# Kernel optimization log

Measured on AMD Instinct MI355X. Metric: run time of the kernel, lower is better.

## Reference

```python
import jax, jax.numpy as jnp
import numpy as np

# Dimensions (LRA BigBird base-ish config)
B, S, D = 4, 4096, 512
H, DH = 8, 64          # num_heads, head_dim = qkv_dim // num_heads
M = 2048               # mlp_dim
BS = 64                # block_size
NB = S // BS           # number of blocks = 64
R = 3                  # num random blocks per row (BigBird default)
K = 8                  # max gathered key blocks per row: 3 window + 2 global + 3 random
SEED = 0               # connectivity_seed
LN_EPS = 1e-6


def _block_indices():
    """Static BigBird connectivity for interior query blocks (rows 1..NB-2).

    Each interior block attends to: window {i-1,i,i+1}, globals {0, NB-1},
    and R random blocks (seeded, disjoint from window/global). Rows where
    window overlaps globals have fewer unique blocks and are padded+masked.
    """
    rng = np.random.RandomState(SEED)
    idx = np.zeros((NB - 2, K), np.int32)
    msk = np.zeros((NB - 2, K), bool)
    for row, i in enumerate(range(1, NB - 1)):
        fixed = sorted({0, NB - 1, i - 1, i, i + 1})
        allowed = [b for b in range(NB) if b not in fixed]
        rand = rng.choice(allowed, size=R, replace=False).tolist()
        blocks = fixed + rand
        idx[row, :len(blocks)] = blocks
        msk[row, :len(blocks)] = True
    return jnp.asarray(idx), jnp.asarray(msk)

IDX, KMASK = _block_indices()  # [NB-2, K] int32 / bool
NEG = -1e9


def _ln(x, scale, bias):
    mu = jnp.mean(x, axis=-1, keepdims=True)
    var = jnp.mean(jnp.square(x - mu), axis=-1, keepdims=True)
    return (x - mu) * jax.lax.rsqrt(var + LN_EPS) * scale + bias


def setup_inputs() -> dict:
    key = jax.random.key(0)
    ks = jax.random.split(key, 7)

    def xav(k, shape, fan_in, fan_out):
        lim = float(np.sqrt(6.0 / (fan_in + fan_out)))
        return jax.random.uniform(k, shape, jnp.float32, -lim, lim)

    return {
        "inputs": jax.random.normal(ks[0], (B, S, D), jnp.float32),
        "ln1_scale": jnp.ones((D,), jnp.float32),
        "ln1_bias": jnp.zeros((D,), jnp.float32),
        "wq": xav(ks[1], (D, H, DH), D, DH),
        "wk": xav(ks[2], (D, H, DH), D, DH),
        "wv": xav(ks[3], (D, H, DH), D, DH),
        "wo": xav(ks[4], (H, DH, D), D, D),
        "ln2_scale": jnp.ones((D,), jnp.float32),
        "ln2_bias": jnp.zeros((D,), jnp.float32),
        "w1": xav(ks[5], (D, M), D, M),
        "b1": jnp.zeros((M,), jnp.float32),
        "w2": xav(ks[6], (M, D), M, D),
        "b2": jnp.zeros((D,), jnp.float32),
    }


def reference(inputs, ln1_scale, ln1_bias, wq, wk, wv, wo,
              ln2_scale, ln2_bias, w1, b1, w2, b2):
    x = _ln(inputs, ln1_scale, ln1_bias)
    scale = 1.0 / jnp.sqrt(jnp.asarray(DH, x.dtype))
    q = jnp.einsum("bsd,dhk->bshk", x, wq) * scale
    k = jnp.einsum("bsd,dhk->bshk", x, wk)
    v = jnp.einsum("bsd,dhk->bshk", x, wv)

    # block layout: [B, H, NB, BS, DH]
    qb = q.reshape(B, NB, BS, H, DH).transpose(0, 3, 1, 2, 4)
    kb = k.reshape(B, NB, BS, H, DH).transpose(0, 3, 1, 2, 4)
    vb = v.reshape(B, NB, BS, H, DH).transpose(0, 3, 1, 2, 4)

    # ---- interior query blocks: sparse (window + global + random) keys ----
    q_int = qb[:, :, 1:NB - 1]                       # [B,H,NB-2,BS,DH]
    k_sel = kb[:, :, IDX]                            # [B,H,NB-2,K,BS,DH]
    v_sel = vb[:, :, IDX]
    s = jnp.einsum("bhnqd,bhnkjd->bhnqkj", q_int, k_sel)
    s = jnp.where(KMASK[None, None, :, None, :, None], s, NEG)
    p = jax.nn.softmax(s.reshape(B, H, NB - 2, BS, K * BS), axis=-1)
    p = p.reshape(B, H, NB - 2, BS, K, BS)
    o_int = jnp.einsum("bhnqkj,bhnkjd->bhnqd", p, v_sel)

    # ---- global query blocks (first & last): full attention ----
    q_g = qb[:, :, jnp.array([0, NB - 1])]           # [B,H,2,BS,DH]
    kf = k.transpose(0, 2, 1, 3)                     # [B,H,S,DH]
    vf = v.transpose(0, 2, 1, 3)
    sg = jnp.einsum("bhgqd,bhtd->bhgqt", q_g, kf)
    pg = jax.nn.softmax(sg, axis=-1)
    o_g = jnp.einsum("bhgqt,bhtd->bhgqd", pg, vf)

    o = jnp.concatenate([o_g[:, :, :1], o_int, o_g[:, :, 1:]], axis=2)
    o = o.transpose(0, 2, 3, 1, 4).reshape(B, S, H, DH)
    attn = jnp.einsum("bshd,hde->bse", o, wo)        # output proj, no bias

    x = attn + inputs                                 # residual 1
    y = _ln(x, ln2_scale, ln2_bias)
    y = jax.nn.gelu(jnp.einsum("bsd,dm->bsm", y, w1) + b1)
    y = jnp.einsum("bsm,md->bsd", y, w2) + b2
    return x + y                                      # residual 2
```

## Files before the change

kernel.cpp:

```cpp
#include <hip/hip_runtime.h>
#include <cstdint>
#include <cstddef>

typedef __bf16 bf16;
typedef __bf16 bf16x8 __attribute__((ext_vector_type(8)));
typedef float  f32x4  __attribute__((ext_vector_type(4)));

#define DEVINL static __device__ __forceinline__

DEVINL void gl2lds16(const void* g, void* l) {
  __builtin_amdgcn_global_load_lds((__attribute__((address_space(1))) void*)g,
                                   (__attribute__((address_space(3))) void*)l,
                                   16, 0, 0);
}

DEVINL float loadf(const void* p, size_t i, int isf) {
  return isf ? ((const float*)p)[i] : (float)((const bf16*)p)[i];
}

DEVINL float gelu_fast(float x) {
  float u = 0.7978845608028654f * (x + 0.044715f * x * x * x);
  float s = 1.f / (1.f + __expf(-2.f * u));
  return x * s;
}

struct TabArg { unsigned char idx[62][8]; unsigned char cnt[62]; };

struct HostMT {
  unsigned mt[624]; int mti;
  void seed(unsigned s) {
    mt[0] = s;
    for (int i = 1; i < 624; ++i) mt[i] = 1812433253u * (mt[i-1] ^ (mt[i-1] >> 30)) + (unsigned)i;
    mti = 624;
  }
  unsigned next() {
    if (mti == 624) {
      for (int i = 0; i < 624; ++i) {
        unsigned y = (mt[i] & 0x80000000u) | (mt[(i+1)%624] & 0x7fffffffu);
        unsigned v = mt[(i+397)%624] ^ (y >> 1);
        if (y & 1u) v ^= 0x9908b0dfu;
        mt[i] = v;
      }
      mti = 0;
    }
    unsigned y = mt[mti++];
    y ^= y >> 11; y ^= (y << 7) & 0x9d2c5680u; y ^= (y << 15) & 0xefc60000u; y ^= y >> 18;
    return y;
  }
  unsigned interval(unsigned mx) {
    if (mx == 0) return 0;
    unsigned mask = mx;
    mask |= mask>>1; mask |= mask>>2; mask |= mask>>4; mask |= mask>>8; mask |= mask>>16;
    unsigned v = next() & mask;
    while (v > mx) v = next() & mask;
    return v;
  }
};

static void build_tab(TabArg* t) {
  HostMT rng; rng.seed(0u);
  for (int row = 0; row < 62; ++row) {
    int i = row + 1;
    bool fix[64] = {};
    fix[0] = true; fix[63] = true; fix[i-1] = true; fix[i] = true; fix[i+1] = true;
    int fixed[5]; int nf = 0; int allowed[64]; int na = 0;
    for (int b = 0; b < 64; ++b) { if (fix[b]) fixed[nf++] = b; else allowed[na++] = b; }
    int perm[64];
    for (int j = 0; j < na; ++j) perm[j] = j;
    for (int j = na - 1; j > 0; --j) {
      unsigned kk = rng.interval((unsigned)j);
      int tmp = perm[j]; perm[j] = perm[kk]; perm[kk] = tmp;
    }
    int nb = 0;
    for (int j = 0; j < nf; ++j) t->idx[row][nb++] = (unsigned char)fixed[j];
    for (int j = 0; j < 3;  ++j) t->idx[row][nb++] = (unsigned char)allowed[perm[j]];
    t->cnt[row] = (unsigned char)nb;
    for (int j = nb; j < 8; ++j) t->idx[row][j] = 0;
  }
}

__global__ __launch_bounds__(256) void detect_kernel(const unsigned short* __restrict__ x,
                                                     int* __restrict__ flag) {
  __shared__ int cnt[256];
  int c = 0;
  for (int i = threadIdx.x; i < 8192; i += 256) {
    int e = (x[i] >> 7) & 0xFF;
    if (e >= 0xC6) c++;
  }
  cnt[threadIdx.x] = c;
  __syncthreads();
  for (int s = 128; s > 0; s >>= 1) {
    if (threadIdx.x < s) cnt[threadIdx.x] += cnt[threadIdx.x + s];
    __syncthreads();
  }
  if (threadIdx.x == 0) *flag = (cnt[0] > 32) ? 1 : 0;
}

struct P6 { const void* s[6]; bf16* d[6]; int n[6]; };
__global__ __launch_bounds__(256) void cvt6_kernel(const int* __restrict__ flagp, P6 p) {
  int isf = *flagp;
  int which = blockIdx.x;
  const void* src = p.s[which];
  bf16* dst = p.d[which];
  int n = p.n[which];
  int i8 = threadIdx.x * 8;
  if (i8 >= n) return;
  bf16x8 o;
  if (isf) {
    const float* s = (const float*)src + i8;
    f32x4 a = *(const f32x4*)s;
    f32x4 b = *(const f32x4*)(s + 4);
#pragma unroll
    for (int j = 0; j < 4; ++j) { o[j] = (bf16)a[j]; o[4+j] = (bf16)b[j]; }
  } else {
    o = *(const bf16x8*)((const bf16*)src + i8);
  }
  *(bf16x8*)(dst + i8) = o;
}

struct W6 { const void* in[6]; bf16* out[6]; int R[6], C[6], start[6]; };
__global__ __launch_bounds__(256) void transpose_w6_kernel(const int* __restrict__ flagp, W6 wz) {
  __shared__ __align__(16) bf16 sT[64 * 72];
  int isf = *flagp;
  int which = 0;
#pragma unroll
  for (int i = 1; i < 6; ++i) if ((int)blockIdx.x >= wz.start[i]) which = i;
  const void* in = wz.in[which];
  bf16* out = wz.out[which];
  int R = wz.R[which], C = wz.C[which];
  int bid = blockIdx.x - wz.start[which];
  int cb = C >> 6;
  int br = bid / cb, bc = bid % cb;
  int r0 = br * 64, c0 = bc * 64;
  int t = threadIdx.x;
#pragma unroll
  for (int p = 0; p < 2; ++p) {
    int cid = p * 256 + t;
    int r = cid >> 3, c = cid & 7;
    bf16x8 v;
    if (isf) {
      const float* s = (const float*)in + (size_t)(r0 + r) * C + c0 + c * 8;
      f32x4 a = *(const f32x4*)s;
      f32x4 b = *(const f32x4*)(s + 4);
#pragma unroll
      for (int j = 0; j < 4; ++j) { v[j] = (bf16)a[j]; v[4+j] = (bf16)b[j]; }
    } else {
      v = *(const bf16x8*)((const bf16*)in + (size_t)(r0 + r) * C + c0 + c * 8);
    }
    *(bf16x8*)&sT[r * 72 + c * 8] = v;
  }
  __syncthreads();
#pragma unroll
  for (int p = 0; p < 2; ++p) {
    int cid = p * 256 + t;
    int oc = cid >> 3, rc = cid & 7;
    bf16x8 vv;
#pragma unroll
    for (int i = 0; i < 8; ++i) vv[i] = sT[(rc * 8 + i) * 72 + oc];
    *(bf16x8*)&out[(size_t)(c0 + oc) * R + r0 + rc * 8] = vv;
  }
}

__global__ __launch_bounds__(256) void ln_any_kernel(const int* __restrict__ flagp,
                                                     const void* __restrict__ x,
                                                     const bf16* __restrict__ sc,
                                                     const bf16* __restrict__ bi,
                                                     bf16* __restrict__ out) {
  int isf = *flagp;
  int row  = blockIdx.x * 4 + (threadIdx.x >> 6);
  int lane = threadIdx.x & 63;
  float f[8];
  if (isf) {
    const float* xf = (const float*)x + (size_t)row * 512 + lane * 8;
    f32x4 a = *(const f32x4*)xf;
    f32x4 b = *(const f32x4*)(xf + 4);
#pragma unroll
    for (int j = 0; j < 4; ++j) { f[j] = a[j]; f[4+j] = b[j]; }
  } else {
    bf16x8 v = ((const bf16x8*)((const bf16*)x + (size_t)row * 512))[lane];
#pragma unroll
    for (int j = 0; j < 8; ++j) f[j] = (float)v[j];
  }
  float s = 0.f, s2 = 0.f;
#pragma unroll
  for (int i = 0; i < 8; ++i) { s += f[i]; s2 += f[i]*f[i]; }
#pragma unroll
  for (int o = 32; o > 0; o >>= 1) { s += __shfl_xor(s, o, 64); s2 += __shfl_xor(s2, o, 64); }
  float mu  = s  * (1.f/512.f);
  float var = s2 * (1.f/512.f) - mu*mu;
  float rs  = rsqrtf(fmaxf(var, 0.f) + 1e-6f);
  bf16x8 sv = ((const bf16x8*)sc)[lane];
  bf16x8 bv = ((const bf16x8*)bi)[lane];
  bf16x8 o8;
#pragma unroll
  for (int i = 0; i < 8; ++i) o8[i] = (bf16)((f[i]-mu)*rs*(float)sv[i] + (float)bv[i]);
  ((bf16x8*)(out + (size_t)row * 512))[lane] = o8;
}

__global__ __launch_bounds__(256) void ln_bf16_kernel(const bf16* __restrict__ x,
                                                      const bf16* __restrict__ sc,
                                                      const bf16* __restrict__ bi,
                                                      bf16* __restrict__ out) {
  int row  = blockIdx.x * 4 + (threadIdx.x >> 6);
  int lane = threadIdx.x & 63;
  bf16x8 v = ((const bf16x8*)(x + (size_t)row * 512))[lane];
  float f[8], s = 0.f, s2 = 0.f;
#pragma unroll
  for (int i = 0; i < 8; ++i) { f[i] = (float)v[i]; s += f[i]; s2 += f[i]*f[i]; }
#pragma unroll
  for (int o = 32; o > 0; o >>= 1) { s += __shfl_xor(s, o, 64); s2 += __shfl_xor(s2, o, 64); }
  float mu  = s  * (1.f/512.f);
  float var = s2 * (1.f/512.f) - mu*mu;
  float rs  = rsqrtf(fmaxf(var, 0.f) + 1e-6f);
  bf16x8 sv = ((const bf16x8*)sc)[lane];
  bf16x8 bv = ((const bf16x8*)bi)[lane];
  bf16x8 o8;
#pragma unroll
  for (int i = 0; i < 8; ++i) o8[i] = (bf16)((f[i]-mu)*rs*(float)sv[i] + (float)bv[i]);
  ((bf16x8*)(out + (size_t)row * 512))[lane] = o8;
}

__global__ __launch_bounds__(256) void transpose_v_kernel(const bf16* __restrict__ v,
                                                          bf16* __restrict__ vT) {
  __shared__ __align__(16) bf16 sT[64 * 72];
  int st = blockIdx.x & 63;
  int h  = (blockIdx.x >> 6) & 7;
  int b  = blockIdx.x >> 9;
  int s0 = st * 64;
  int t  = threadIdx.x;
  const size_t ibase = ((size_t)b * 4096) * 512 + h * 64;
#pragma unroll
  for (int p = 0; p < 2; ++p) {
    int cid = p * 256 + t;
    int r = cid >> 3, c = cid & 7;
    *(bf16x8*)&sT[r * 72 + c * 8] = *(const bf16x8*)&v[ibase + (size_t)(s0 + r) * 512 + c * 8];
  }
  __syncthreads();
  const size_t obase = ((size_t)(b * 8 + h) * 64) * 4096;
#pragma unroll
  for (int p = 0; p < 2; ++p) {
    int cid = p * 256 + t;
    int dh = cid >> 3, scn = cid & 7;
    bf16x8 vv;
#pragma unroll
    for (int i = 0; i < 8; ++i) vv[i] = sT[(scn * 8 + i) * 72 + dh];
    *(bf16x8*)&vT[obase + (size_t)dh * 4096 + s0 + scn * 8] = vv;
  }
}

__global__ __launch_bounds__(256) void gemm_kernel(const bf16* __restrict__ A,
                                                   const bf16* __restrict__ BT,
                                                   int M, int N, int K,
                                                   int epi,
                                                   const bf16* __restrict__ bias,
                                                   const void* __restrict__ resid,
                                                   void* __restrict__ gout,
                                                   bf16* __restrict__ out2,
                                                   bf16* __restrict__ out3,
                                                   size_t gout_off,
                                                   const int* __restrict__ flagp) {
  __shared__ __align__(16) bf16 As[128 * 64];
  __shared__ __align__(16) bf16 Bs[128 * 64];
  const int t = threadIdx.x;
  const int w = t >> 6, l = t & 63, quad = l >> 4, l15 = l & 15;
  const int wm = w >> 1, wn = w & 1;
  const int m0 = blockIdx.y * 128, n0 = blockIdx.x * 128;
  const int isf = (epi == 1 || epi == 3) ? *flagp : 0;
  f32x4 acc[4][4] = {};
  const int nk = K >> 6;
  for (int kt = 0; kt < nk; ++kt) {
    __syncthreads();
#pragma unroll
    for (int p = 0; p < 4; ++p) {
      int cid = p * 256 + t;
      int r = cid >> 3, c = cid & 7;
      int sc_ = c ^ (r & 7);
      gl2lds16(A  + (size_t)(m0 + r) * K + kt * 64 + sc_ * 8, (char*)As + cid * 16);
      gl2lds16(BT + (size_t)(n0 + r) * K + kt * 64 + sc_ * 8, (char*)Bs + cid * 16);
    }
    __syncthreads();
#pragma unroll
    for (int ks = 0; ks < 2; ++ks) {
      bf16x8 af[4], bfr[4];
      int cc = ks * 4 + quad;
#pragma unroll
      for (int mt = 0; mt < 4; ++mt) {
        int r = wm * 64 + mt * 16 + l15;
        af[mt] = *(const bf16x8*)&As[r * 64 + ((cc ^ (r & 7)) << 3)];
      }
#pragma unroll
      for (int nt = 0; nt < 4; ++nt) {
        int r = wn * 64 + nt * 16 + l15;
        bfr[nt] = *(const bf16x8*)&Bs[r * 64 + ((cc ^ (r & 7)) << 3)];
      }
#pragma unroll
      for (int mt = 0; mt < 4; ++mt)
#pragma unroll
        for (int nt = 0; nt < 4; ++nt)
          acc[mt][nt] = __builtin_amdgcn_mfma_f32_16x16x32_bf16(af[mt], bfr[nt], acc[mt][nt], 0, 0, 0);
    }
  }
#pragma unroll
  for (int mt = 0; mt < 4; ++mt) {
    int rowb = m0 + wm * 64 + mt * 16 + quad * 4;
#pragma unroll
    for (int nt = 0; nt < 4; ++nt) {
      int col = n0 + wn * 64 + nt * 16 + l15;
#pragma unroll
      for (int r = 0; r < 4; ++r) {
        int row = rowb + r;
        float vacc = acc[mt][nt][r];
        size_t oidx = (size_t)row * N + col;
        if (epi == 5) {
          int which = col >> 9, c2 = col & 511;
          bf16 ov = (bf16)(which == 0 ? vacc * 0.125f : vacc);
          bf16* dst = which == 0 ? (bf16*)gout : (which == 1 ? out2 : out3);
          dst[(size_t)row * 512 + c2] = ov;
        } else if (epi == 1) {
          ((bf16*)gout)[oidx] = (bf16)(vacc + loadf(resid, oidx, isf));
        } else if (epi == 2) {
          ((bf16*)gout)[oidx] = (bf16)gelu_fast(vacc + (float)bias[col]);
        } else {
          float v = vacc + (float)bias[col] + (float)((const bf16*)resid)[oidx];
          if (isf) ((float*)gout)[gout_off + oidx] = v;
          else     ((bf16*)gout)[gout_off + oidx] = (bf16)v;
        }
      }
    }
  }
}

__global__ __launch_bounds__(256) void attn_kernel(TabArg targ,
                                                   const bf16* __restrict__ q,
                                                   const bf16* __restrict__ k,
                                                   const bf16* __restrict__ vT,
                                                   bf16* __restrict__ o,
                                                   float* __restrict__ part,
                                                   int mode) {
  __shared__ __align__(16) bf16 sQ[64 * 64];
  __shared__ __align__(16) bf16 sK[64 * 64];
  __shared__ __align__(16) bf16 sV[64 * 64];
  __shared__ __align__(16) bf16 sP[64 * 64];

  const int t = threadIdx.x;
  const int w = t >> 6, l = t & 63, quad = l >> 4, l15 = l & 15;
  int n, bh, chunk = 0, niter;
  if (mode == 0) {
    n = 1 + (int)(blockIdx.x % 62);
    bh = blockIdx.x / 62;
    niter = (int)targ.cnt[n - 1];
  } else {
    chunk = blockIdx.x & 7;
    int g = (blockIdx.x >> 3) & 1;
    bh = blockIdx.x >> 4;
    n = g ? 63 : 0;
    niter = 8;
  }
  const int b = bh >> 3, h = bh & 7;
  const size_t bh_qk = ((size_t)b * 4096) * 512 + h * 64;
  const size_t bh_v  = ((size_t)(b * 8 + h) * 64) * 4096;

#pragma unroll
  for (int p = 0; p < 2; ++p) {
    int cid = p * 256 + t;
    int r = cid >> 3, c = cid & 7;
    int sc_ = c ^ (r & 7);
    gl2lds16(q + bh_qk + (size_t)(n * 64 + r) * 512 + sc_ * 8, (char*)sQ + cid * 16);
  }

  float m_r[4], l_r[4];
#pragma unroll
  for (int r = 0; r < 4; ++r) { m_r[r] = -1e30f; l_r[r] = 0.f; }
  f32x4 accO[4] = {};

  for (int it = 0; it < niter; ++it) {
    int kb = (mode == 0) ? (int)targ.idx[n - 1][it] : chunk * 8 + it;
    __syncthreads();
#pragma unroll
    for (int p = 0; p < 2; ++p) {
      int cid = p * 256 + t;
      int r = cid >> 3, c = cid & 7;
      int sc_ = c ^ (r & 7);
      gl2lds16(k  + bh_qk + (size_t)(kb * 64 + r) * 512 + sc_ * 8, (char*)sK + cid * 16);
      gl2lds16(vT + bh_v  + (size_t)r * 4096 + kb * 64 + sc_ * 8,  (char*)sV + cid * 16);
    }
    __syncthreads();

    f32x4 accS[4] = {};
#pragma unroll
    for (int ks = 0; ks < 2; ++ks) {
      int rQ = w * 16 + l15;
      int cc = ks * 4 + quad;
      bf16x8 afr = *(const bf16x8*)&sQ[rQ * 64 + ((cc ^ (rQ & 7)) << 3)];
#pragma unroll
      for (int j = 0; j < 4; ++j) {
        int rK = j * 16 + l15;
        bf16x8 bfr = *(const bf16x8*)&sK[rK * 64 + ((cc ^ (rK & 7)) << 3)];
        accS[j] = __builtin_amdgcn_mfma_f32_16x16x32_bf16(afr, bfr, accS[j], 0, 0, 0);
      }
    }

    float al[4];
#pragma unroll
    for (int r = 0; r < 4; ++r) {
      float mx = fmaxf(fmaxf(accS[0][r], accS[1][r]), fmaxf(accS[2][r], accS[3][r]));
#pragma unroll
      for (int off = 1; off < 16; off <<= 1) mx = fmaxf(mx, __shfl_xor(mx, off, 64));
      float mnew = fmaxf(m_r[r], mx);
      al[r] = __expf(m_r[r] - mnew);
      m_r[r] = mnew;
      int rowp = w * 16 + quad * 4 + r;
      float ps = 0.f;
#pragma unroll
      for (int j = 0; j < 4; ++j) {
        float pv = __expf(accS[j][r] - mnew);
        ps += pv;
        int col = j * 16 + l15;
        sP[rowp * 64 + (((col >> 3) ^ (rowp & 7)) << 3) + (col & 7)] = (bf16)pv;
      }
#pragma unroll
      for (int off = 1; off < 16; off <<= 1) ps += __shfl_xor(ps, off, 64);
      l_r[r] = l_r[r] * al[r] + ps;
    }

#pragma unroll
    for (int dt = 0; dt < 4; ++dt)
#pragma unroll
      for (int r = 0; r < 4; ++r) accO[dt][r] *= al[r];
#pragma unroll
    for (int ks = 0; ks < 2; ++ks) {
      int rP = w * 16 + l15;
      int cc = ks * 4 + quad;
      bf16x8 afr = *(const bf16x8*)&sP[rP * 64 + ((cc ^ (rP & 7)) << 3)];
#pragma unroll
      for (int dt = 0; dt < 4; ++dt) {
        int rV = dt * 16 + l15;
        bf16x8 bfr = *(const bf16x8*)&sV[rV * 64 + ((cc ^ (rV & 7)) << 3)];
        accO[dt] = __builtin_amdgcn_mfma_f32_16x16x32_bf16(afr, bfr, accO[dt], 0, 0, 0);
      }
    }
  }

  if (mode == 0) {
#pragma unroll
    for (int r = 0; r < 4; ++r) {
      int qr = w * 16 + quad * 4 + r;
      float linv = 1.f / fmaxf(l_r[r], 1e-30f);
      int srow = n * 64 + qr;
#pragma unroll
      for (int dt = 0; dt < 4; ++dt)
        o[bh_qk + (size_t)srow * 512 + dt * 16 + l15] = (bf16)(accO[dt][r] * linv);
    }
  } else {
    float* pb = part + (size_t)blockIdx.x * (4096 + 128);
#pragma unroll
    for (int r = 0; r < 4; ++r) {
      int row = w * 16 + quad * 4 + r;
#pragma unroll
      for (int dt = 0; dt < 4; ++dt)
        pb[row * 64 + dt * 16 + l15] = accO[dt][r];
      if (l15 == 0) { pb[4096 + row] = m_r[r]; pb[4160 + row] = l_r[r]; }
    }
  }
}

__global__ __launch_bounds__(256) void merge_kernel(const float* __restrict__ part,
                                                    bf16* __restrict__ o) {
  const int SP = 4096 + 128;
  int g = blockIdx.x & 1, bh = blockIdx.x >> 1;
  int b = bh >> 3, h = bh & 7, n = g ? 63 : 0;
  int t = threadIdx.x;
  int row = t >> 2, st = t & 3;
  size_t pb0 = (size_t)(bh * 16 + g * 8) * SP;
  float mc[8], lc[8], M = -1e30f;
#pragma unroll
  for (int c = 0; c < 8; ++c) {
    mc[c] = part[pb0 + (size_t)c * SP + 4096 + row];
    lc[c] = part[pb0 + (size_t)c * SP + 4160 + row];
    M = fmaxf(M, mc[c]);
  }
  float L = 0.f;
  float sc[8];
#pragma unroll
  for (int c = 0; c < 8; ++c) { sc[c] = __expf(mc[c] - M); L += lc[c] * sc[c]; }
  float inv = 1.f / fmaxf(L, 1e-30f);
  f32x4 acc[4] = {};
#pragma unroll
  for (int c = 0; c < 8; ++c) {
    const float* Op = part + pb0 + (size_t)c * SP + row * 64 + st * 16;
    float s = sc[c];
#pragma unroll
    for (int i = 0; i < 4; ++i) {
      f32x4 v = *(const f32x4*)(Op + i * 4);
#pragma unroll
      for (int j = 0; j < 4; ++j) acc[i][j] += v[j] * s;
    }
  }
  size_t obase = ((size_t)b * 4096 + n * 64 + row) * 512 + h * 64 + st * 16;
#pragma unroll
  for (int i = 0; i < 4; ++i)
#pragma unroll
    for (int j = 0; j < 4; ++j)
      o[obase + i * 4 + j] = (bf16)(acc[i][j] * inv);
}

extern "C" void kernel_launch(void* const* d_in, const int* in_sizes, int n_in,
                              void* d_out, int out_size, void* d_ws, size_t ws_size,
                              hipStream_t stream) {
  (void)in_sizes; (void)n_in; (void)out_size;
  const void* inputs = d_in[0];
  const void* ln1s = d_in[1];
  const void* ln1b = d_in[2];
  const void* wq   = d_in[3];
  const void* wk   = d_in[4];
  const void* wv   = d_in[5];
  const void* wo   = d_in[6];
  const void* ln2s = d_in[7];
  const void* ln2b = d_in[8];
  const void* w1   = d_in[9];
  const void* b1   = d_in[10];
  const void* w2   = d_in[11];
  const void* b2   = d_in[12];

  TabArg tab;
  build_tab(&tab);

  char* ws = (char*)d_ws;
  size_t off = 0;
  auto alloc = [&](size_t bytes) -> char* {
    char* p = ws + off; off += (bytes + 255) & ~(size_t)255; return p;
  };
  int*  flag   = (int*)alloc(256);
  bf16* ln1s_c = (bf16*)alloc(512 * 2);
  bf16* ln1b_c = (bf16*)alloc(512 * 2);
  bf16* ln2s_c = (bf16*)alloc(512 * 2);
  bf16* ln2b_c = (bf16*)alloc(512 * 2);
  bf16* b1_c   = (bf16*)alloc(2048 * 2);
  bf16* b2_c   = (bf16*)alloc(512 * 2);
  bf16* wqkvT  = (bf16*)alloc(1536ull * 512 * 2);
  bf16* woT    = (bf16*)alloc(512ull * 512 * 2);
  bf16* w1T    = (bf16*)alloc(512ull * 2048 * 2);
  bf16* w2T    = (bf16*)alloc(2048ull * 512 * 2);
  const size_t SZ = 16384ull * 512 * 2;
  bf16* regA = (bf16*)alloc(SZ);
  bf16* regB = (bf16*)alloc(SZ);
  bf16* regC = (bf16*)alloc(SZ);
  bf16* regD = (bf16*)alloc(SZ);
  size_t base_need = off;
  const size_t H1_BYTES = 16384ull * 2048 * 2;
  bool full_ffn = (ws_size >= base_need + H1_BYTES + 256);
  bf16* h1f = full_ffn ? (bf16*)alloc(H1_BYTES) : nullptr;

  bf16* xln  = regA;
  bf16* qb   = regB;
  bf16* kb   = regC;
  bf16* vb   = regD;
  bf16* vTb  = regA;
  bf16* obuf = regD;
  bf16* xbuf = regA;
  bf16* yln  = regB;
  bf16* h1c  = regC;
  float* part = (float*)d_out;

  detect_kernel<<<1, 256, 0, stream>>>((const unsigned short*)inputs, flag);

  P6 p6;
  p6.s[0]=ln1s; p6.s[1]=ln1b; p6.s[2]=ln2s; p6.s[3]=ln2b; p6.s[4]=b1; p6.s[5]=b2;
  p6.d[0]=ln1s_c; p6.d[1]=ln1b_c; p6.d[2]=ln2s_c; p6.d[3]=ln2b_c; p6.d[4]=b1_c; p6.d[5]=b2_c;
  p6.n[0]=512; p6.n[1]=512; p6.n[2]=512; p6.n[3]=512; p6.n[4]=2048; p6.n[5]=512;
  cvt6_kernel<<<6, 256, 0, stream>>>(flag, p6);

  W6 w6;
  w6.in[0]=wq; w6.in[1]=wk; w6.in[2]=wv; w6.in[3]=wo; w6.in[4]=w1; w6.in[5]=w2;
  w6.out[0]=wqkvT; w6.out[1]=wqkvT+512ull*512; w6.out[2]=wqkvT+1024ull*512;
  w6.out[3]=woT; w6.out[4]=w1T; w6.out[5]=w2T;
  w6.R[0]=512; w6.R[1]=512; w6.R[2]=512; w6.R[3]=512; w6.R[4]=512;  w6.R[5]=2048;
  w6.C[0]=512; w6.C[1]=512; w6.C[2]=512; w6.C[3]=512; w6.C[4]=2048; w6.C[5]=512;
  w6.start[0]=0; w6.start[1]=64; w6.start[2]=128; w6.start[3]=192; w6.start[4]=256; w6.start[5]=512;
  transpose_w6_kernel<<<768, 256, 0, stream>>>(flag, w6);

  ln_any_kernel<<<4096, 256, 0, stream>>>(flag, inputs, ln1s_c, ln1b_c, xln);

  gemm_kernel<<<dim3(12, 128), 256, 0, stream>>>(xln, wqkvT, 16384, 1536, 512, 5,
                                                 nullptr, nullptr, qb, kb, vb, 0, flag);

  transpose_v_kernel<<<2048, 256, 0, stream>>>(vb, vTb);

  attn_kernel<<<1984, 256, 0, stream>>>(tab, qb, kb, vTb, obuf, part, 0);
  attn_kernel<<<512,  256, 0, stream>>>(tab, qb, kb, vTb, obuf, part, 1);
  merge_kernel<<<64,  256, 0, stream>>>(part, obuf);

  gemm_kernel<<<dim3(4, 128), 256, 0, stream>>>(obuf, woT, 16384, 512, 512, 1,
                                                nullptr, inputs, xbuf, nullptr, nullptr, 0, flag);

  ln_bf16_kernel<<<4096, 256, 0, stream>>>(xbuf, ln2s_c, ln2b_c, yln);

  if (full_ffn) {
    gemm_kernel<<<dim3(16, 128), 256, 0, stream>>>(yln, w1T, 16384, 2048, 512, 2,
                                                   b1_c, nullptr, h1f, nullptr, nullptr, 0, flag);
    gemm_kernel<<<dim3(4, 128), 256, 0, stream>>>(h1f, w2T, 16384, 512, 2048, 3,
                                                  b2_c, xbuf, d_out, nullptr, nullptr, 0, flag);
  } else {
    for (int c = 0; c < 4; ++c) {
      const bf16* yc = yln  + (size_t)c * 4096 * 512;
      const bf16* xc = xbuf + (size_t)c * 4096 * 512;
      size_t oo = (size_t)c * 4096 * 512;
      gemm_kernel<<<dim3(16, 32), 256, 0, stream>>>(yc, w1T, 4096, 2048, 512, 2,
                                                    b1_c, nullptr, h1c, nullptr, nullptr, 0, flag);
      gemm_kernel<<<dim3(4, 32), 256, 0, stream>>>(h1c, w2T, 4096, 512, 2048, 3,
                                                   b2_c, xc, d_out, nullptr, nullptr, oo, flag);
    }
  }
}
```

Before: 479.6 us.

## Stage GEMM epilogue through LDS for vectorized stores and XCD-aware block mapping

```diff
diff --git a/kernel.cpp b/kernel.cpp
--- a/kernel.cpp
+++ b/kernel.cpp
@@ -12,10 +12,6 @@
   __builtin_amdgcn_global_load_lds((__attribute__((address_space(1))) void*)g,
                                    (__attribute__((address_space(3))) void*)l,
                                    16, 0, 0);
-}
-
-DEVINL float loadf(const void* p, size_t i, int isf) {
-  return isf ? ((const float*)p)[i] : (float)((const bf16*)p)[i];
 }
 
 DEVINL float gelu_fast(float x) {
@@ -250,7 +246,7 @@
 
 __global__ __launch_bounds__(256) void gemm_kernel(const bf16* __restrict__ A,
                                                    const bf16* __restrict__ BT,
-                                                   int M, int N, int K,
+                                                   int N, int K, int nbn,
                                                    int epi,
                                                    const bf16* __restrict__ bias,
                                                    const void* __restrict__ resid,
@@ -259,12 +255,15 @@
                                                    bf16* __restrict__ out3,
                                                    size_t gout_off,
                                                    const int* __restrict__ flagp) {
-  __shared__ __align__(16) bf16 As[128 * 64];
-  __shared__ __align__(16) bf16 Bs[128 * 64];
+  __shared__ __align__(16) bf16 smem[2 * 128 * 64];
+  bf16* As = smem;
+  bf16* Bs = smem + 128 * 64;
   const int t = threadIdx.x;
   const int w = t >> 6, l = t & 63, quad = l >> 4, l15 = l & 15;
   const int wm = w >> 1, wn = w & 1;
-  const int m0 = blockIdx.y * 128, n0 = blockIdx.x * 128;
+  const int xcd = blockIdx.x & 7, g = blockIdx.x >> 3;
+  const int m0 = (xcd + (g / nbn) * 8) * 128;
+  const int n0 = (g % nbn) * 128;
   const int isf = (epi == 1 || epi == 3) ? *flagp : 0;
   f32x4 acc[4][4] = {};
   const int nk = K >> 6;
@@ -300,30 +299,73 @@
           acc[mt][nt] = __builtin_amdgcn_mfma_f32_16x16x32_bf16(af[mt], bfr[nt], acc[mt][nt], 0, 0, 0);
     }
   }
-#pragma unroll
-  for (int mt = 0; mt < 4; ++mt) {
-    int rowb = m0 + wm * 64 + mt * 16 + quad * 4;
-#pragma unroll
-    for (int nt = 0; nt < 4; ++nt) {
-      int col = n0 + wn * 64 + nt * 16 + l15;
-#pragma unroll
-      for (int r = 0; r < 4; ++r) {
-        int row = rowb + r;
-        float vacc = acc[mt][nt][r];
-        size_t oidx = (size_t)row * N + col;
-        if (epi == 5) {
-          int which = col >> 9, c2 = col & 511;
-          bf16 ov = (bf16)(which == 0 ? vacc * 0.125f : vacc);
-          bf16* dst = which == 0 ? (bf16*)gout : (which == 1 ? out2 : out3);
-          dst[(size_t)row * 512 + c2] = ov;
-        } else if (epi == 1) {
-          ((bf16*)gout)[oidx] = (bf16)(vacc + loadf(resid, oidx, isf));
-        } else if (epi == 2) {
-          ((bf16*)gout)[oidx] = (bf16)gelu_fast(vacc + (float)bias[col]);
+
+  const int ESTR = 144;
+  for (int half = 0; half < 2; ++half) {
+    __syncthreads();
+    if (wm == half) {
+#pragma unroll
+      for (int mt = 0; mt < 4; ++mt) {
+        int lr = mt * 16 + quad * 4;
+#pragma unroll
+        for (int nt = 0; nt < 4; ++nt) {
+          int col = wn * 64 + nt * 16 + l15;
+#pragma unroll
+          for (int r = 0; r < 4; ++r) {
+            float v = acc[mt][nt][r];
+            bf16 ov;
+            if (epi == 5)      ov = (bf16)(((n0 + col) >> 9) == 0 ? v * 0.125f : v);
+            else if (epi == 2) ov = (bf16)gelu_fast(v + (float)bias[n0 + col]);
+            else if (epi == 3) ov = (bf16)(v + (float)bias[n0 + col]);
+            else               ov = (bf16)v;
+            smem[(lr + r) * ESTR + col] = ov;
+          }
+        }
+      }
+    }
+    __syncthreads();
+    int gr0 = m0 + half * 64;
+#pragma unroll
+    for (int it = 0; it < 4; ++it) {
+      int cid = it * 256 + t;
+      int lr  = cid >> 4;
+      int c8  = (cid & 15) * 8;
+      bf16x8 vv = *(const bf16x8*)&smem[lr * ESTR + c8];
+      int grow = gr0 + lr;
+      int gcol = n0 + c8;
+      size_t oidx = (size_t)grow * N + gcol;
+      if (epi == 5) {
+        int which = gcol >> 9, c2 = gcol & 511;
+        bf16* dst = which == 0 ? (bf16*)gout : (which == 1 ? out2 : out3);
+        *(bf16x8*)&dst[(size_t)grow * 512 + c2] = vv;
+      } else if (epi == 1) {
+        bf16x8 ov;
+        if (isf) {
+          const float* rp = (const float*)resid + oidx;
+          f32x4 a = *(const f32x4*)rp, b = *(const f32x4*)(rp + 4);
+#pragma unroll
+          for (int j = 0; j < 4; ++j) { ov[j] = (bf16)((float)vv[j] + a[j]); ov[4+j] = (bf16)((float)vv[4+j] + b[j]); }
         } else {
-          float v = vacc + (float)bias[col] + (float)((const bf16*)resid)[oidx];
-          if (isf) ((float*)gout)[gout_off + oidx] = v;
-          else     ((bf16*)gout)[gout_off + oidx] = (bf16)v;
+          bf16x8 rv = *(const bf16x8*)((const bf16*)resid + oidx);
+#pragma unroll
+          for (int j = 0; j < 8; ++j) ov[j] = (bf16)((float)vv[j] + (float)rv[j]);
+        }
+        *(bf16x8*)&((bf16*)gout)[oidx] = ov;
+      } else if (epi == 2) {
+        *(bf16x8*)&((bf16*)gout)[oidx] = vv;
+      } else {
+        bf16x8 rv = *(const bf16x8*)((const bf16*)resid + oidx);
+        if (isf) {
+          float o0[8];
+#pragma unroll
+          for (int j = 0; j < 8; ++j) o0[j] = (float)vv[j] + (float)rv[j];
+          *(f32x4*)&((float*)gout)[gout_off + oidx]     = *(f32x4*)&o0[0];
+          *(f32x4*)&((float*)gout)[gout_off + oidx + 4] = *(f32x4*)&o0[4];
+        } else {
+          bf16x8 ov;
+#pragma unroll
+          for (int j = 0; j < 8; ++j) ov[j] = (bf16)((float)vv[j] + (float)rv[j]);
+          *(bf16x8*)&((bf16*)gout)[gout_off + oidx] = ov;
         }
       }
     }
@@ -346,8 +388,10 @@
   const int w = t >> 6, l = t & 63, quad = l >> 4, l15 = l & 15;
   int n, bh, chunk = 0, niter;
   if (mode == 0) {
-    n = 1 + (int)(blockIdx.x % 62);
-    bh = blockIdx.x / 62;
+    int xcd = blockIdx.x & 7, g = blockIdx.x >> 3;
+    int bhloc = g / 62;
+    n  = 1 + g % 62;
+    bh = xcd + bhloc * 8;
     niter = (int)targ.cnt[n - 1];
   } else {
     chunk = blockIdx.x & 7;
@@ -581,8 +625,8 @@
 
   ln_any_kernel<<<4096, 256, 0, stream>>>(flag, inputs, ln1s_c, ln1b_c, xln);
 
-  gemm_kernel<<<dim3(12, 128), 256, 0, stream>>>(xln, wqkvT, 16384, 1536, 512, 5,
-                                                 nullptr, nullptr, qb, kb, vb, 0, flag);
+  gemm_kernel<<<128 * 12, 256, 0, stream>>>(xln, wqkvT, 1536, 512, 12, 5,
+                                            nullptr, nullptr, qb, kb, vb, 0, flag);
 
   transpose_v_kernel<<<2048, 256, 0, stream>>>(vb, vTb);
 
@@ -590,25 +634,25 @@
   attn_kernel<<<512,  256, 0, stream>>>(tab, qb, kb, vTb, obuf, part, 1);
   merge_kernel<<<64,  256, 0, stream>>>(part, obuf);
 
-  gemm_kernel<<<dim3(4, 128), 256, 0, stream>>>(obuf, woT, 16384, 512, 512, 1,
-                                                nullptr, inputs, xbuf, nullptr, nullptr, 0, flag);
+  gemm_kernel<<<128 * 4, 256, 0, stream>>>(obuf, woT, 512, 512, 4, 1,
+                                           nullptr, inputs, xbuf, nullptr, nullptr, 0, flag);
 
   ln_bf16_kernel<<<4096, 256, 0, stream>>>(xbuf, ln2s_c, ln2b_c, yln);
 
   if (full_ffn) {
-    gemm_kernel<<<dim3(16, 128), 256, 0, stream>>>(yln, w1T, 16384, 2048, 512, 2,
-                                                   b1_c, nullptr, h1f, nullptr, nullptr, 0, flag);
-    gemm_kernel<<<dim3(4, 128), 256, 0, stream>>>(h1f, w2T, 16384, 512, 2048, 3,
-                                                  b2_c, xbuf, d_out, nullptr, nullptr, 0, flag);
+    gemm_kernel<<<128 * 16, 256, 0, stream>>>(yln, w1T, 2048, 512, 16, 2,
+                                              b1_c, nullptr, h1f, nullptr, nullptr, 0, flag);
+    gemm_kernel<<<128 * 4, 256, 0, stream>>>(h1f, w2T, 512, 2048, 4, 3,
+                                             b2_c, xbuf, d_out, nullptr, nullptr, 0, flag);
   } else {
     for (int c = 0; c < 4; ++c) {
       const bf16* yc = yln  + (size_t)c * 4096 * 512;
       const bf16* xc = xbuf + (size_t)c * 4096 * 512;
       size_t oo = (size_t)c * 4096 * 512;
-      gemm_kernel<<<dim3(16, 32), 256, 0, stream>>>(yc, w1T, 4096, 2048, 512, 2,
-                                                    b1_c, nullptr, h1c, nullptr, nullptr, 0, flag);
-      gemm_kernel<<<dim3(4, 32), 256, 0, stream>>>(h1c, w2T, 4096, 512, 2048, 3,
-                                                   b2_c, xc, d_out, nullptr, nullptr, oo, flag);
-    }
-  }
-}
+      gemm_kernel<<<32 * 16, 256, 0, stream>>>(yc, w1T, 2048, 512, 16, 2,
+                                               b1_c, nullptr, h1c, nullptr, nullptr, 0, flag);
+      gemm_kernel<<<32 * 4, 256, 0, stream>>>(h1c, w2T, 512, 2048, 4, 3,
+                                              b2_c, xc, d_out, nullptr, nullptr, oo, flag);
+    }
+  }
+}
```

After: 485.1 us. No clear change (+1.1%).

## Double-buffer GEMM LDS tiles and remap blocks to group work per XCD

Applied to the files above, without the earlier changes.

```diff
diff --git a/kernel.cpp b/kernel.cpp
--- a/kernel.cpp
+++ b/kernel.cpp
@@ -250,7 +250,7 @@
 
 __global__ __launch_bounds__(256) void gemm_kernel(const bf16* __restrict__ A,
                                                    const bf16* __restrict__ BT,
-                                                   int M, int N, int K,
+                                                   int N, int K, int nbn,
                                                    int epi,
                                                    const bf16* __restrict__ bias,
                                                    const void* __restrict__ resid,
@@ -259,26 +259,43 @@
                                                    bf16* __restrict__ out3,
                                                    size_t gout_off,
                                                    const int* __restrict__ flagp) {
-  __shared__ __align__(16) bf16 As[128 * 64];
-  __shared__ __align__(16) bf16 Bs[128 * 64];
+  __shared__ __align__(16) bf16 As[2][128 * 64];
+  __shared__ __align__(16) bf16 Bs[2][128 * 64];
   const int t = threadIdx.x;
   const int w = t >> 6, l = t & 63, quad = l >> 4, l15 = l & 15;
   const int wm = w >> 1, wn = w & 1;
-  const int m0 = blockIdx.y * 128, n0 = blockIdx.x * 128;
+  const int xcd = blockIdx.x & 7, g = blockIdx.x >> 3;
+  const int m0 = (xcd + (g / nbn) * 8) * 128;
+  const int n0 = (g % nbn) * 128;
   const int isf = (epi == 1 || epi == 3) ? *flagp : 0;
   f32x4 acc[4][4] = {};
   const int nk = K >> 6;
+
+  const int sr = t >> 1;
+  (void)sr;
+
+#pragma unroll
+  for (int p = 0; p < 4; ++p) {
+    int cid = p * 256 + t;
+    int r = cid >> 3, c = cid & 7;
+    int sc_ = c ^ (r & 7);
+    gl2lds16(A  + (size_t)(m0 + r) * K + sc_ * 8, (char*)As[0] + cid * 16);
+    gl2lds16(BT + (size_t)(n0 + r) * K + sc_ * 8, (char*)Bs[0] + cid * 16);
+  }
+
   for (int kt = 0; kt < nk; ++kt) {
     __syncthreads();
-#pragma unroll
-    for (int p = 0; p < 4; ++p) {
-      int cid = p * 256 + t;
-      int r = cid >> 3, c = cid & 7;
-      int sc_ = c ^ (r & 7);
-      gl2lds16(A  + (size_t)(m0 + r) * K + kt * 64 + sc_ * 8, (char*)As + cid * 16);
-      gl2lds16(BT + (size_t)(n0 + r) * K + kt * 64 + sc_ * 8, (char*)Bs + cid * 16);
-    }
-    __syncthreads();
+    int nb = (kt + 1) & 1, cb = kt & 1;
+    if (kt + 1 < nk) {
+#pragma unroll
+      for (int p = 0; p < 4; ++p) {
+        int cid = p * 256 + t;
+        int r = cid >> 3, c = cid & 7;
+        int sc_ = c ^ (r & 7);
+        gl2lds16(A  + (size_t)(m0 + r) * K + (kt + 1) * 64 + sc_ * 8, (char*)As[nb] + cid * 16);
+        gl2lds16(BT + (size_t)(n0 + r) * K + (kt + 1) * 64 + sc_ * 8, (char*)Bs[nb] + cid * 16);
+      }
+    }
 #pragma unroll
     for (int ks = 0; ks < 2; ++ks) {
       bf16x8 af[4], bfr[4];
@@ -286,12 +303,12 @@
 #pragma unroll
       for (int mt = 0; mt < 4; ++mt) {
         int r = wm * 64 + mt * 16 + l15;
-        af[mt] = *(const bf16x8*)&As[r * 64 + ((cc ^ (r & 7)) << 3)];
+        af[mt] = *(const bf16x8*)&As[cb][r * 64 + ((cc ^ (r & 7)) << 3)];
       }
 #pragma unroll
       for (int nt = 0; nt < 4; ++nt) {
         int r = wn * 64 + nt * 16 + l15;
-        bfr[nt] = *(const bf16x8*)&Bs[r * 64 + ((cc ^ (r & 7)) << 3)];
+        bfr[nt] = *(const bf16x8*)&Bs[cb][r * 64 + ((cc ^ (r & 7)) << 3)];
       }
 #pragma unroll
       for (int mt = 0; mt < 4; ++mt)
@@ -300,6 +317,7 @@
           acc[mt][nt] = __builtin_amdgcn_mfma_f32_16x16x32_bf16(af[mt], bfr[nt], acc[mt][nt], 0, 0, 0);
     }
   }
+
 #pragma unroll
   for (int mt = 0; mt < 4; ++mt) {
     int rowb = m0 + wm * 64 + mt * 16 + quad * 4;
@@ -346,8 +364,10 @@
   const int w = t >> 6, l = t & 63, quad = l >> 4, l15 = l & 15;
   int n, bh, chunk = 0, niter;
   if (mode == 0) {
-    n = 1 + (int)(blockIdx.x % 62);
-    bh = blockIdx.x / 62;
+    int xcd = blockIdx.x & 7, g = blockIdx.x >> 3;
+    int bhloc = g / 62;
+    n  = 1 + g % 62;
+    bh = xcd + bhloc * 8;
     niter = (int)targ.cnt[n - 1];
   } else {
     chunk = blockIdx.x & 7;
@@ -581,8 +601,8 @@
 
   ln_any_kernel<<<4096, 256, 0, stream>>>(flag, inputs, ln1s_c, ln1b_c, xln);
 
-  gemm_kernel<<<dim3(12, 128), 256, 0, stream>>>(xln, wqkvT, 16384, 1536, 512, 5,
-                                                 nullptr, nullptr, qb, kb, vb, 0, flag);
+  gemm_kernel<<<128 * 12, 256, 0, stream>>>(xln, wqkvT, 1536, 512, 12, 5,
+                                            nullptr, nullptr, qb, kb, vb, 0, flag);
 
   transpose_v_kernel<<<2048, 256, 0, stream>>>(vb, vTb);
 
@@ -590,25 +610,25 @@
   attn_kernel<<<512,  256, 0, stream>>>(tab, qb, kb, vTb, obuf, part, 1);
   merge_kernel<<<64,  256, 0, stream>>>(part, obuf);
 
-  gemm_kernel<<<dim3(4, 128), 256, 0, stream>>>(obuf, woT, 16384, 512, 512, 1,
-                                                nullptr, inputs, xbuf, nullptr, nullptr, 0, flag);
+  gemm_kernel<<<128 * 4, 256, 0, stream>>>(obuf, woT, 512, 512, 4, 1,
+                                           nullptr, inputs, xbuf, nullptr, nullptr, 0, flag);
 
   ln_bf16_kernel<<<4096, 256, 0, stream>>>(xbuf, ln2s_c, ln2b_c, yln);
 
   if (full_ffn) {
-    gemm_kernel<<<dim3(16, 128), 256, 0, stream>>>(yln, w1T, 16384, 2048, 512, 2,
-                                                   b1_c, nullptr, h1f, nullptr, nullptr, 0, flag);
-    gemm_kernel<<<dim3(4, 128), 256, 0, stream>>>(h1f, w2T, 16384, 512, 2048, 3,
-                                                  b2_c, xbuf, d_out, nullptr, nullptr, 0, flag);
+    gemm_kernel<<<128 * 16, 256, 0, stream>>>(yln, w1T, 2048, 512, 16, 2,
+                                              b1_c, nullptr, h1f, nullptr, nullptr, 0, flag);
+    gemm_kernel<<<128 * 4, 256, 0, stream>>>(h1f, w2T, 512, 2048, 4, 3,
+                                             b2_c, xbuf, d_out, nullptr, nullptr, 0, flag);
   } else {
     for (int c = 0; c < 4; ++c) {
       const bf16* yc = yln  + (size_t)c * 4096 * 512;
       const bf16* xc = xbuf + (size_t)c * 4096 * 512;
       size_t oo = (size_t)c * 4096 * 512;
-      gemm_kernel<<<dim3(16, 32), 256, 0, stream>>>(yc, w1T, 4096, 2048, 512, 2,
-                                                    b1_c, nullptr, h1c, nullptr, nullptr, 0, flag);
-      gemm_kernel<<<dim3(4, 32), 256, 0, stream>>>(h1c, w2T, 4096, 512, 2048, 3,
-                                                   b2_c, xc, d_out, nullptr, nullptr, oo, flag);
-    }
-  }
-}
+      gemm_kernel<<<32 * 16, 256, 0, stream>>>(yc, w1T, 2048, 512, 16, 2,
+                                               b1_c, nullptr, h1c, nullptr, nullptr, 0, flag);
+      gemm_kernel<<<32 * 4, 256, 0, stream>>>(h1c, w2T, 512, 2048, 4, 3,
+                                              b2_c, xc, d_out, nullptr, nullptr, oo, flag);
+    }
+  }
+}
```

After: 453.5 us. 1.06x faster.

## Replace tiled GEMM with row-panel GEMM streaming weights from global; XCD-swizzle attention

Applied to the files above, without the earlier changes.

```diff
diff --git a/kernel.cpp b/kernel.cpp
--- a/kernel.cpp
+++ b/kernel.cpp
@@ -248,85 +248,99 @@
   }
 }
 
-__global__ __launch_bounds__(256) void gemm_kernel(const bf16* __restrict__ A,
-                                                   const bf16* __restrict__ BT,
-                                                   int M, int N, int K,
-                                                   int epi,
-                                                   const bf16* __restrict__ bias,
-                                                   const void* __restrict__ resid,
-                                                   void* __restrict__ gout,
-                                                   bf16* __restrict__ out2,
-                                                   bf16* __restrict__ out3,
-                                                   size_t gout_off,
-                                                   const int* __restrict__ flagp) {
-  __shared__ __align__(16) bf16 As[128 * 64];
-  __shared__ __align__(16) bf16 Bs[128 * 64];
+__global__ __launch_bounds__(512) void gemmA_kernel(const bf16* __restrict__ A,
+                                                    const bf16* __restrict__ BT,
+                                                    int N, int K, int epi,
+                                                    const bf16* __restrict__ bias,
+                                                    const void* __restrict__ resid,
+                                                    void* __restrict__ gout,
+                                                    bf16* __restrict__ out2,
+                                                    bf16* __restrict__ out3,
+                                                    size_t gout_off,
+                                                    const int* __restrict__ flagp) {
+  __shared__ __align__(16) bf16 sA[64 * 512];
   const int t = threadIdx.x;
   const int w = t >> 6, l = t & 63, quad = l >> 4, l15 = l & 15;
-  const int wm = w >> 1, wn = w & 1;
-  const int m0 = blockIdx.y * 128, n0 = blockIdx.x * 128;
+  const int wm = w & 3, wn = w >> 2;
+  const int m0 = blockIdx.x * 64;
   const int isf = (epi == 1 || epi == 3) ? *flagp : 0;
-  f32x4 acc[4][4] = {};
-  const int nk = K >> 6;
-  for (int kt = 0; kt < nk; ++kt) {
-    __syncthreads();
-#pragma unroll
-    for (int p = 0; p < 4; ++p) {
-      int cid = p * 256 + t;
-      int r = cid >> 3, c = cid & 7;
-      int sc_ = c ^ (r & 7);
-      gl2lds16(A  + (size_t)(m0 + r) * K + kt * 64 + sc_ * 8, (char*)As + cid * 16);
-      gl2lds16(BT + (size_t)(n0 + r) * K + kt * 64 + sc_ * 8, (char*)Bs + cid * 16);
-    }
-    __syncthreads();
-#pragma unroll
-    for (int ks = 0; ks < 2; ++ks) {
-      bf16x8 af[4], bfr[4];
-      int cc = ks * 4 + quad;
-#pragma unroll
-      for (int mt = 0; mt < 4; ++mt) {
-        int r = wm * 64 + mt * 16 + l15;
-        af[mt] = *(const bf16x8*)&As[r * 64 + ((cc ^ (r & 7)) << 3)];
+  const int rr = wm * 16 + l15;
+
+  auto stage = [&](int kc) {
+#pragma unroll
+    for (int p = 0; p < 8; ++p) {
+      int cid = p * 512 + t;
+      int r = cid >> 6, c = cid & 63;
+      int sc = c ^ (r & 7);
+      gl2lds16(A + (size_t)(m0 + r) * K + kc * 512 + sc * 8, (char*)sA + cid * 16);
+    }
+  };
+
+  auto compute_group = [&](int g, int kc, f32x4* acc) {
+    const int n0g = g * 128 + wn * 64;
+    const bf16* bp = BT + (size_t)(n0g + l15) * K + (size_t)kc * 512 + quad * 8;
+#pragma unroll
+    for (int ks = 0; ks < 16; ++ks) {
+      int kidx = ks * 4 + quad;
+      bf16x8 af = *(const bf16x8*)&sA[rr * 512 + ((kidx ^ (rr & 7)) << 3)];
+#pragma unroll
+      for (int nt = 0; nt < 4; ++nt) {
+        bf16x8 bf = *(const bf16x8*)(bp + (size_t)nt * 16 * K + ks * 32);
+        acc[nt] = __builtin_amdgcn_mfma_f32_16x16x32_bf16(af, bf, acc[nt], 0, 0, 0);
       }
-#pragma unroll
-      for (int nt = 0; nt < 4; ++nt) {
-        int r = wn * 64 + nt * 16 + l15;
-        bfr[nt] = *(const bf16x8*)&Bs[r * 64 + ((cc ^ (r & 7)) << 3)];
-      }
-#pragma unroll
-      for (int mt = 0; mt < 4; ++mt)
-#pragma unroll
-        for (int nt = 0; nt < 4; ++nt)
-          acc[mt][nt] = __builtin_amdgcn_mfma_f32_16x16x32_bf16(af[mt], bfr[nt], acc[mt][nt], 0, 0, 0);
-    }
-  }
-#pragma unroll
-  for (int mt = 0; mt < 4; ++mt) {
-    int rowb = m0 + wm * 64 + mt * 16 + quad * 4;
+    }
+  };
+
+  auto store_group = [&](int g, f32x4* acc) {
+    const int n0g = g * 128 + wn * 64;
+    const int rowb = m0 + wm * 16 + quad * 4;
 #pragma unroll
     for (int nt = 0; nt < 4; ++nt) {
-      int col = n0 + wn * 64 + nt * 16 + l15;
+      int col = n0g + nt * 16 + l15;
 #pragma unroll
       for (int r = 0; r < 4; ++r) {
         int row = rowb + r;
-        float vacc = acc[mt][nt][r];
+        float v = acc[nt][r];
         size_t oidx = (size_t)row * N + col;
         if (epi == 5) {
           int which = col >> 9, c2 = col & 511;
-          bf16 ov = (bf16)(which == 0 ? vacc * 0.125f : vacc);
+          bf16 ov = (bf16)(which == 0 ? v * 0.125f : v);
           bf16* dst = which == 0 ? (bf16*)gout : (which == 1 ? out2 : out3);
           dst[(size_t)row * 512 + c2] = ov;
         } else if (epi == 1) {
-          ((bf16*)gout)[oidx] = (bf16)(vacc + loadf(resid, oidx, isf));
+          ((bf16*)gout)[oidx] = (bf16)(v + loadf(resid, oidx, isf));
         } else if (epi == 2) {
-          ((bf16*)gout)[oidx] = (bf16)gelu_fast(vacc + (float)bias[col]);
+          ((bf16*)gout)[oidx] = (bf16)gelu_fast(v + (float)bias[col]);
         } else {
-          float v = vacc + (float)bias[col] + (float)((const bf16*)resid)[oidx];
-          if (isf) ((float*)gout)[gout_off + oidx] = v;
-          else     ((bf16*)gout)[gout_off + oidx] = (bf16)v;
+          float ov = v + (float)bias[col] + (float)((const bf16*)resid)[oidx];
+          if (isf) ((float*)gout)[gout_off + oidx] = ov;
+          else     ((bf16*)gout)[gout_off + oidx] = (bf16)ov;
         }
       }
     }
+  };
+
+  if (epi != 3) {
+    stage(0);
+    __syncthreads();
+    const int ng = N >> 7;
+    for (int g = 0; g < ng; ++g) {
+      f32x4 acc[4] = {};
+      compute_group(g, 0, acc);
+      store_group(g, acc);
+    }
+  } else {
+    f32x4 accA[4][4] = {};
+    const int nkc = K >> 9;
+    for (int kc = 0; kc < nkc; ++kc) {
+      __syncthreads();
+      stage(kc);
+      __syncthreads();
+#pragma unroll
+      for (int g = 0; g < 4; ++g) compute_group(g, kc, accA[g]);
+    }
+#pragma unroll
+    for (int g = 0; g < 4; ++g) store_group(g, accA[g]);
   }
 }
 
@@ -346,8 +360,10 @@
   const int w = t >> 6, l = t & 63, quad = l >> 4, l15 = l & 15;
   int n, bh, chunk = 0, niter;
   if (mode == 0) {
-    n = 1 + (int)(blockIdx.x % 62);
-    bh = blockIdx.x / 62;
+    int xcd = blockIdx.x & 7, g = blockIdx.x >> 3;
+    int bhloc = g / 62;
+    n  = 1 + g % 62;
+    bh = xcd + bhloc * 8;
     niter = (int)targ.cnt[n - 1];
   } else {
     chunk = blockIdx.x & 7;
@@ -581,8 +597,8 @@
 
   ln_any_kernel<<<4096, 256, 0, stream>>>(flag, inputs, ln1s_c, ln1b_c, xln);
 
-  gemm_kernel<<<dim3(12, 128), 256, 0, stream>>>(xln, wqkvT, 16384, 1536, 512, 5,
-                                                 nullptr, nullptr, qb, kb, vb, 0, flag);
+  gemmA_kernel<<<256, 512, 0, stream>>>(xln, wqkvT, 1536, 512, 5,
+                                        nullptr, nullptr, qb, kb, vb, 0, flag);
 
   transpose_v_kernel<<<2048, 256, 0, stream>>>(vb, vTb);
 
@@ -590,25 +606,25 @@
   attn_kernel<<<512,  256, 0, stream>>>(tab, qb, kb, vTb, obuf, part, 1);
   merge_kernel<<<64,  256, 0, stream>>>(part, obuf);
 
-  gemm_kernel<<<dim3(4, 128), 256, 0, stream>>>(obuf, woT, 16384, 512, 512, 1,
-                                                nullptr, inputs, xbuf, nullptr, nullptr, 0, flag);
+  gemmA_kernel<<<256, 512, 0, stream>>>(obuf, woT, 512, 512, 1,
+                                        nullptr, inputs, xbuf, nullptr, nullptr, 0, flag);
 
   ln_bf16_kernel<<<4096, 256, 0, stream>>>(xbuf, ln2s_c, ln2b_c, yln);
 
   if (full_ffn) {
-    gemm_kernel<<<dim3(16, 128), 256, 0, stream>>>(yln, w1T, 16384, 2048, 512, 2,
-                                                   b1_c, nullptr, h1f, nullptr, nullptr, 0, flag);
-    gemm_kernel<<<dim3(4, 128), 256, 0, stream>>>(h1f, w2T, 16384, 512, 2048, 3,
-                                                  b2_c, xbuf, d_out, nullptr, nullptr, 0, flag);
+    gemmA_kernel<<<256, 512, 0, stream>>>(yln, w1T, 2048, 512, 2,
+                                          b1_c, nullptr, h1f, nullptr, nullptr, 0, flag);
+    gemmA_kernel<<<256, 512, 0, stream>>>(h1f, w2T, 512, 2048, 3,
+                                          b2_c, xbuf, d_out, nullptr, nullptr, 0, flag);
   } else {
     for (int c = 0; c < 4; ++c) {
       const bf16* yc = yln  + (size_t)c * 4096 * 512;
       const bf16* xc = xbuf + (size_t)c * 4096 * 512;
       size_t oo = (size_t)c * 4096 * 512;
-      gemm_kernel<<<dim3(16, 32), 256, 0, stream>>>(yc, w1T, 4096, 2048, 512, 2,
-                                                    b1_c, nullptr, h1c, nullptr, nullptr, 0, flag);
-      gemm_kernel<<<dim3(4, 32), 256, 0, stream>>>(h1c, w2T, 4096, 512, 2048, 3,
-                                                   b2_c, xc, d_out, nullptr, nullptr, oo, flag);
-    }
-  }
-}
+      gemmA_kernel<<<64, 512, 0, stream>>>(yc, w1T, 2048, 512, 2,
+                                           b1_c, nullptr, h1c, nullptr, nullptr, 0, flag);
+      gemmA_kernel<<<64, 512, 0, stream>>>(h1c, w2T, 512, 2048, 3,
+                                           b2_c, xc, d_out, nullptr, nullptr, oo, flag);
+    }
+  }
+}
```

New measurement: 1.138 ms. 137% more time.
